# Performance work log

Measured on AMD Instinct MI355X. Metric: run time of the kernel, lower is better.

Reference implementation:

```python
import jax, jax.numpy as jnp
import numpy as np

BETA = 0.95
THR = 1.0
NUM_STEPS = 25
NUM_IN, NUM_HID, NUM_OUT = 9, 100, 2
BATCH = 65536


def _heaviside(x):
    return (x > 0).astype(x.dtype)


def setup_inputs() -> dict:
    key = jax.random.key(0)
    ks = jax.random.split(key, 5)
    x = jax.random.normal(ks[0], (BATCH, NUM_IN), dtype=jnp.float32)
    # nn.Linear default init: U(-1/sqrt(fan_in), 1/sqrt(fan_in))
    b1lim = 1.0 / np.sqrt(NUM_IN)
    b2lim = 1.0 / np.sqrt(NUM_HID)
    W1 = jax.random.uniform(ks[1], (NUM_HID, NUM_IN), jnp.float32, -b1lim, b1lim)
    b1 = jax.random.uniform(ks[2], (NUM_HID,), jnp.float32, -b1lim, b1lim)
    W2 = jax.random.uniform(ks[3], (NUM_OUT, NUM_HID), jnp.float32, -b2lim, b2lim)
    b2 = jax.random.uniform(ks[4], (NUM_OUT,), jnp.float32, -b2lim, b2lim)
    return {"x": x, "W1": W1, "b1": b1, "W2": W2, "b2": b2}


def reference(x, W1, b1, W2, b2):
    # cur1 = fc1(x) is identical every step (x is static) -> hoist out of loop
    cur1 = x @ W1.T + b1                     # [B, 100]
    mem1 = jnp.zeros((x.shape[0], NUM_HID), x.dtype)
    mem2 = jnp.zeros((x.shape[0], NUM_OUT), x.dtype)

    def step(carry, _):
        mem1, mem2 = carry
        # snntorch Leaky, reset_mechanism='subtract': reset from PREVIOUS mem
        reset1 = _heaviside(mem1 - THR)
        mem1 = BETA * mem1 + cur1 - reset1 * THR
        spk1 = _heaviside(mem1 - THR)        # [B, 100]
        cur2 = spk1 @ W2.T + b2              # [B, 2]
        reset2 = _heaviside(mem2 - THR)
        mem2 = BETA * mem2 + cur2 - reset2 * THR
        return (mem1, mem2), mem2

    (_, _), mem2_rec = jax.lax.scan(step, (mem1, mem2), None, length=NUM_STEPS)
    return mem2_rec                          # [25, B, 2]
```

## Files before the change

### kernel.cpp

```cpp
#include <hip/hip_runtime.h>

#define BATCH  65536
#define NIN    9
#define NHID   100
#define TSTEPS 25
#define CHUNK  5
#define EPS    3e-5f

typedef float v2f __attribute__((ext_vector_type(2)));

__global__ __launch_bounds__(256, 4) void snn_kernel(
    const float* __restrict__ x,  const float* __restrict__ W1,
    const float* __restrict__ b1, const float* __restrict__ W2,
    const float* __restrict__ b2, float* __restrict__ out)
{
    __shared__ float sx[64 * NIN];
    __shared__ v2f   sacc[2][4][CHUNK][64];

    const int tid  = threadIdx.x;
    const int lane = tid & 63;
    const int wq   = __builtin_amdgcn_readfirstlane(tid >> 6);
    const int b0   = blockIdx.x * 64;

    for (int i = tid; i < 64 * NIN; i += 256) sx[i] = x[(size_t)b0 * NIN + i];
    __syncthreads();

    float xv[NIN];
#pragma unroll
    for (int i = 0; i < NIN; ++i) xv[i] = sx[lane * NIN + i];

    float a0[TSTEPS], a1[TSTEPS];
#pragma unroll
    for (int t = 0; t < TSTEPS; ++t) { a0[t] = 0.f; a1[t] = 0.f; }

    const int h0 = wq * 25;
#pragma unroll 1
    for (int j = 0; j < 25; ++j) {
        const int h = h0 + j;
        float c32 = 0.f;
#pragma unroll
        for (int i = 0; i < NIN; ++i) c32 = fmaf(W1[h * NIN + i], xv[i], c32);
        c32 += b1[h];
        const float k  = c32 - 0.05f;
        const float k1 = c32 - 1.05f;
        const float w0 = W2[h], w1 = W2[NHID + h];

        float u = -1.0f, ming = 1e30f;
        bool  s = false;
#pragma unroll
        for (int t = 0; t < TSTEPS; ++t) {
            u = fmaf(0.95f, u, s ? k1 : k);
            s = (u > 0.0f);
            ming = fminf(ming, fabsf(u));
            float d = s ? 1.f : 0.f;
            asm("v_fmac_f32 %0, %1, %2" : "+v"(a0[t]) : "s"(w0), "v"(d));
            asm("v_fmac_f32 %0, %1, %2" : "+v"(a1[t]) : "s"(w1), "v"(d));
        }

        if (__any(ming < EPS)) {
            double c64 = 0.0;
#pragma unroll
            for (int i = 0; i < NIN; ++i)
                c64 += (double)W1[h * NIN + i] * (double)xv[i];
            c64 += (double)b1[h];
            const double c1 = c64 - 1.0;

            double md = 0.0;  bool sd = false;
            float  ur = -1.0f; bool sr = false;
#pragma unroll
            for (int t = 0; t < TSTEPS; ++t) {
                ur = fmaf(0.95f, ur, sr ? k1 : k);
                sr = (ur > 0.0f);
                md = 0.95 * md + (sd ? c1 : c64);
                sd = (md > 1.0);
                if (sr != sd) {
                    float sg = sd ? 1.f : -1.f;
                    a0[t] = fmaf(sg, w0, a0[t]);
                    a1[t] = fmaf(sg, w1, a1[t]);
                }
            }
        }
    }

    double m20 = 0.0, m21 = 0.0;
    double bb0 = (double)b2[0], bb1 = (double)b2[1];

#pragma unroll
    for (int k = 0; k < TSTEPS / CHUNK; ++k) {
#pragma unroll
        for (int u = 0; u < CHUNK; ++u)
            sacc[k & 1][wq][u][lane] = (v2f){a0[k * CHUNK + u], a1[k * CHUNK + u]};
        __syncthreads();
        if (wq == 0) {
#pragma unroll
            for (int u = 0; u < CHUNK; ++u) {
                const int t = k * CHUNK + u;
                v2f q0 = sacc[k & 1][0][u][lane];
                v2f q1 = sacc[k & 1][1][u][lane];
                v2f q2 = sacc[k & 1][2][u][lane];
                v2f q3 = sacc[k & 1][3][u][lane];
                v2f sum = (q0 + q1) + (q2 + q3);
                double r0 = (m20 > 1.0) ? 1.0 : 0.0;
                double r1 = (m21 > 1.0) ? 1.0 : 0.0;
                m20 = 0.95 * m20 + ((double)sum[0] + bb0) - r0;
                m21 = 0.95 * m21 + ((double)sum[1] + bb1) - r1;
                *(float2*)(out + ((size_t)t * BATCH + b0 + lane) * 2) =
                    make_float2((float)m20, (float)m21);
            }
        }
    }
}

extern "C" void kernel_launch(void* const* d_in, const int* in_sizes, int n_in,
                              void* d_out, int out_size, void* d_ws, size_t ws_size,
                              hipStream_t stream) {
    const float* x  = (const float*)d_in[0];
    const float* W1 = (const float*)d_in[1];
    const float* b1 = (const float*)d_in[2];
    const float* W2 = (const float*)d_in[3];
    const float* b2 = (const float*)d_in[4];
    float* out = (float*)d_out;

    dim3 grid(BATCH / 64), block(256);
    hipLaunchKernelGGL(snn_kernel, grid, block, 0, stream, x, W1, b1, W2, b2, out);
}
```

Before: 98.79 us.

## Software-pipeline weight loads across hidden units and defer fp64 fixup pass

Unrolls the hidden-unit loop by two and prefetches the next unit's W1/b1/W2 values into registers while the current unit's 25-step recurrence runs, so global load latency is hidden. The inline asm fmac with SGPR operands is replaced by plain fmaf. The per-unit fp64 correction check is turned into a bitmask and run in a separate pass after the main loop, keeping the hot loop free of branches. The cost is extra registers for the double-buffered weights and a second reload of weights for units that need correction.

```diff
diff --git a/kernel.cpp b/kernel.cpp
--- a/kernel.cpp
+++ b/kernel.cpp
@@ -34,30 +34,67 @@
     for (int t = 0; t < TSTEPS; ++t) { a0[t] = 0.f; a1[t] = 0.f; }
 
     const int h0 = wq * 25;
+    unsigned int badmask = 0;
+
+#define SNN_BODY(J, WR, BV, W0, W1V)                                         \
+    {                                                                        \
+        float c32 = 0.f;                                                     \
+        _Pragma("unroll")                                                    \
+        for (int i = 0; i < NIN; ++i) c32 = fmaf((WR)[i], xv[i], c32);       \
+        c32 += (BV);                                                         \
+        const float k  = c32 - 0.05f;                                        \
+        const float k1 = c32 - 1.05f;                                        \
+        float u = -1.0f, ming = 1e30f;                                       \
+        bool  s = false;                                                     \
+        _Pragma("unroll")                                                    \
+        for (int t = 0; t < TSTEPS; ++t) {                                   \
+            u = fmaf(0.95f, u, s ? k1 : k);                                  \
+            s = (u > 0.0f);                                                  \
+            ming = fminf(ming, fabsf(u));                                    \
+            const float d = s ? 1.f : 0.f;                                   \
+            a0[t] = fmaf(d, (W0), a0[t]);                                    \
+            a1[t] = fmaf(d, (W1V), a1[t]);                                   \
+        }                                                                    \
+        badmask |= __any(ming < EPS) ? (1u << (J)) : 0u;                     \
+    }
+
+    float WrA[NIN], WrB[NIN];
+    float b1A, w0A, w1A, b1B, w0B, w1B;
+#pragma unroll
+    for (int i = 0; i < NIN; ++i) WrA[i] = W1[h0 * NIN + i];
+    b1A = b1[h0]; w0A = W2[h0]; w1A = W2[NHID + h0];
+
 #pragma unroll 1
-    for (int j = 0; j < 25; ++j) {
-        const int h = h0 + j;
-        float c32 = 0.f;
+    for (int jj = 0; jj < 24; jj += 2) {
+        const int hB = h0 + jj + 1;
 #pragma unroll
-        for (int i = 0; i < NIN; ++i) c32 = fmaf(W1[h * NIN + i], xv[i], c32);
-        c32 += b1[h];
-        const float k  = c32 - 0.05f;
-        const float k1 = c32 - 1.05f;
-        const float w0 = W2[h], w1 = W2[NHID + h];
+        for (int i = 0; i < NIN; ++i) WrB[i] = W1[hB * NIN + i];
+        b1B = b1[hB]; w0B = W2[hB]; w1B = W2[NHID + hB];
 
-        float u = -1.0f, ming = 1e30f;
-        bool  s = false;
+        SNN_BODY(jj, WrA, b1A, w0A, w1A)
+
+        const int hA = h0 + jj + 2;
 #pragma unroll
-        for (int t = 0; t < TSTEPS; ++t) {
-            u = fmaf(0.95f, u, s ? k1 : k);
-            s = (u > 0.0f);
-            ming = fminf(ming, fabsf(u));
-            float d = s ? 1.f : 0.f;
-            asm("v_fmac_f32 %0, %1, %2" : "+v"(a0[t]) : "s"(w0), "v"(d));
-            asm("v_fmac_f32 %0, %1, %2" : "+v"(a1[t]) : "s"(w1), "v"(d));
-        }
+        for (int i = 0; i < NIN; ++i) WrA[i] = W1[hA * NIN + i];
+        b1A = b1[hA]; w0A = W2[hA]; w1A = W2[NHID + hA];
 
-        if (__any(ming < EPS)) {
+        SNN_BODY(jj + 1, WrB, b1B, w0B, w1B)
+    }
+    SNN_BODY(24, WrA, b1A, w0A, w1A)
+#undef SNN_BODY
+
+    if (badmask) {
+#pragma unroll 1
+        for (int j = 0; j < 25; ++j) {
+            if (!((badmask >> j) & 1u)) continue;
+            const int h = h0 + j;
+            float c32 = 0.f;
+#pragma unroll
+            for (int i = 0; i < NIN; ++i) c32 = fmaf(W1[h * NIN + i], xv[i], c32);
+            c32 += b1[h];
+            const float k  = c32 - 0.05f;
+            const float k1 = c32 - 1.05f;
+            const float w0 = W2[h], w1 = W2[NHID + h];
             double c64 = 0.0;
 #pragma unroll
             for (int i = 0; i < NIN; ++i)
@@ -65,8 +102,8 @@
             c64 += (double)b1[h];
             const double c1 = c64 - 1.0;
 
-            double md = 0.0;  bool sd = false;
             float  ur = -1.0f; bool sr = false;
+            double md = 0.0;   bool sd = false;
 #pragma unroll
             for (int t = 0; t < TSTEPS; ++t) {
                 ur = fmaf(0.95f, ur, sr ? k1 : k);
@@ -74,7 +111,7 @@
                 md = 0.95 * md + (sd ? c1 : c64);
                 sd = (md > 1.0);
                 if (sr != sd) {
-                    float sg = sd ? 1.f : -1.f;
+                    const float sg = sd ? 1.f : -1.f;
                     a0[t] = fmaf(sg, w0, a0[t]);
                     a1[t] = fmaf(sg, w1, a1[t]);
                 }
```

Result: slower. 103.1 us (+4.3%).
